# Kernel optimization log

Hardware: AMD Instinct MI355X
Metric: run time of the kernel (lower is better)

The kernel has to match this reference:

```python
import jax, jax.numpy as jnp
import numpy as np

D_MODEL = 1024
NUM_HEADS = 16
D_K = D_MODEL // NUM_HEADS


def setup_inputs() -> dict:
    key = jax.random.key(0)
    ks = jax.random.split(key, 11)
    B, S = 2, 2048
    scale = 1.0 / np.sqrt(D_MODEL)
    inp = {
        'Q': jax.random.normal(ks[0], (B, S, D_MODEL), dtype=jnp.float32),
        'K': jax.random.normal(ks[1], (B, S, D_MODEL), dtype=jnp.float32),
        'V': jax.random.normal(ks[2], (B, S, D_MODEL), dtype=jnp.float32),
        'Wq': jax.random.normal(ks[3], (D_MODEL, D_MODEL), dtype=jnp.float32) * scale,
        'bq': jax.random.normal(ks[4], (D_MODEL,), dtype=jnp.float32) * scale,
        'Wk': jax.random.normal(ks[5], (D_MODEL, D_MODEL), dtype=jnp.float32) * scale,
        'bk': jax.random.normal(ks[6], (D_MODEL,), dtype=jnp.float32) * scale,
        'Wv': jax.random.normal(ks[7], (D_MODEL, D_MODEL), dtype=jnp.float32) * scale,
        'bv': jax.random.normal(ks[8], (D_MODEL,), dtype=jnp.float32) * scale,
        'Wo': jax.random.normal(ks[9], (D_MODEL, D_MODEL), dtype=jnp.float32) * scale,
        'bo': jax.random.normal(ks[10], (D_MODEL,), dtype=jnp.float32) * scale,
    }
    return inp


def _split_heads(x):
    B, S, _ = x.shape
    return x.reshape(B, S, NUM_HEADS, D_K).transpose(0, 2, 1, 3)  # [B,H,S,dk]


def reference(Q, K, V, Wq, bq, Wk, bk, Wv, bv, Wo, bo):
    # Linear projections (torch Linear: x @ W.T + b)
    q = _split_heads(Q @ Wq.T + bq)
    k = _split_heads(K @ Wk.T + bk)
    v = _split_heads(V @ Wv.T + bv)
    scores = jnp.einsum('bhqd,bhkd->bhqk', q, k) / jnp.sqrt(jnp.float32(D_K))
    probs = jax.nn.softmax(scores, axis=-1)
    out = jnp.einsum('bhqk,bhkd->bhqd', probs, v)  # [B,H,S,dk]
    B, H, S, dk = out.shape
    out = out.transpose(0, 2, 1, 3).reshape(B, S, D_MODEL)
    return out @ Wo.T + bo
```

## Files before the change

### kernel.cpp

```cpp
#include <hip/hip_runtime.h>
#include <hip/hip_bf16.h>

#define DEV __device__ __forceinline__

#define BATCH 2
#define SEQ   2048
#define DMODEL 1024
#define NHEAD 16
#define DK    64
#define MROWS (BATCH*SEQ)
#define KD    1024
#define GEMM_NT (KD/32)

#define QSCALE 0.18033688011112042f
#define SMREF  17.312340490667560f

typedef __attribute__((ext_vector_type(4))) float f32x4;
typedef __attribute__((ext_vector_type(8))) short s16x8;
typedef __attribute__((ext_vector_type(4))) short s16x4;
typedef __attribute__((ext_vector_type(4))) float fvec4;

__device__ short g_X[3][MROWS*DMODEL];
__device__ short g_W[4][DMODEL*DMODEL];
__device__ short g_q [MROWS*DMODEL];
__device__ short g_k [MROWS*DMODEL];
__device__ short g_vt[MROWS*DMODEL];
__device__ short g_at[MROWS*DMODEL];

DEV short f2bf(float f) {
  union { __hip_bfloat16 h; short s; } u;
  u.h = __float2bfloat16(f);
  return u.s;
}

DEV void gload_lds16(const void* g, void* l) {
  __builtin_amdgcn_global_load_lds(
      (const __attribute__((address_space(1))) void*)g,
      (__attribute__((address_space(3))) void*)l, 16, 0, 0);
}

__global__ __launch_bounds__(256) void cast3(const float* __restrict__ a,
                                             const float* __restrict__ b,
                                             const float* __restrict__ c, int n8) {
  const float* src = blockIdx.z == 0 ? a : blockIdx.z == 1 ? b : c;
  short* dst = g_X[blockIdx.z];
  int i = blockIdx.x * 256 + threadIdx.x;
  if (i < n8) {
    const fvec4* p = (const fvec4*)(src + (size_t)i*8);
    fvec4 v0 = p[0], v1 = p[1];
    s16x8 r;
    r[0]=f2bf(v0[0]); r[1]=f2bf(v0[1]); r[2]=f2bf(v0[2]); r[3]=f2bf(v0[3]);
    r[4]=f2bf(v1[0]); r[5]=f2bf(v1[1]); r[6]=f2bf(v1[2]); r[7]=f2bf(v1[3]);
    *(s16x8*)(dst + (size_t)i*8) = r;
  }
}

__global__ __launch_bounds__(256) void cast4(const float* __restrict__ a,
                                             const float* __restrict__ b,
                                             const float* __restrict__ c,
                                             const float* __restrict__ d, int n8) {
  const float* src = blockIdx.z == 0 ? a : blockIdx.z == 1 ? b
                   : blockIdx.z == 2 ? c : d;
  short* dst = g_W[blockIdx.z];
  int i = blockIdx.x * 256 + threadIdx.x;
  if (i < n8) {
    const fvec4* p = (const fvec4*)(src + (size_t)i*8);
    fvec4 v0 = p[0], v1 = p[1];
    s16x8 r;
    r[0]=f2bf(v0[0]); r[1]=f2bf(v0[1]); r[2]=f2bf(v0[2]); r[3]=f2bf(v0[3]);
    r[4]=f2bf(v1[0]); r[5]=f2bf(v1[1]); r[6]=f2bf(v1[2]); r[7]=f2bf(v1[3]);
    *(s16x8*)(dst + (size_t)i*8) = r;
  }
}

struct GemmSmem { short As[3][128*32]; short Bs[3][128*32]; };

DEV void gemm_core(GemmSmem& sm, const short* __restrict__ A,
                   const short* __restrict__ Bw, const float* __restrict__ bias,
                   void* __restrict__ outp, float scale, int mode,
                   int rowBase, int colBase) {
  const int t = threadIdx.x, l = t & 63, w = t >> 6, g = l >> 4;
  const int wr = w >> 1, wc = w & 1;

  f32x4 acc[4][4] = {};

  auto stage = [&](int buf, int k0) {
#pragma unroll
    for (int j = 0; j < 2; ++j) {
      int e = w*1024 + j*512 + l*8;
      int e2 = e ^ (((e >> 7) & 3) << 3);
      int r = e2 >> 5, c = e2 & 31;
      gload_lds16(A  + (size_t)(rowBase + r)*KD + k0 + c, &sm.As[buf][w*1024 + j*512]);
      gload_lds16(Bw + (size_t)(colBase + r)*KD + k0 + c, &sm.Bs[buf][w*1024 + j*512]);
    }
  };

  stage(0, 0);
  stage(1, 32);

  int cur = 0, nxt = 2;
  for (int i = 0; i < GEMM_NT; ++i) {
    if (i < GEMM_NT - 1) asm volatile("s_waitcnt vmcnt(4)" ::: "memory");
    else                 asm volatile("s_waitcnt vmcnt(0)" ::: "memory");
    __builtin_amdgcn_s_barrier();
    __builtin_amdgcn_sched_barrier(0);

    s16x8 a[4], b[4];
#pragma unroll
    for (int x = 0; x < 4; ++x) {
      int ra = wr*64 + x*16 + (l & 15);
      int ia = (ra*32 + g*8) ^ (((ra >> 2) & 3) << 3);
      a[x] = *(const s16x8*)&sm.As[cur][ia];
      int rb = wc*64 + x*16 + (l & 15);
      int ib = (rb*32 + g*8) ^ (((rb >> 2) & 3) << 3);
      b[x] = *(const s16x8*)&sm.Bs[cur][ib];
    }
    if (i + 2 < GEMM_NT) stage(nxt, (i + 2)*32);
    __builtin_amdgcn_sched_barrier(0);

    __builtin_amdgcn_s_setprio(1);
#pragma unroll
    for (int x = 0; x < 4; ++x)
#pragma unroll
      for (int jn = 0; jn < 4; ++jn)
        acc[x][jn] = __builtin_amdgcn_mfma_f32_16x16x32_bf16(a[x], b[jn], acc[x][jn], 0, 0, 0);
    __builtin_amdgcn_s_setprio(0);

    cur = cur == 2 ? 0 : cur + 1;
    nxt = nxt == 2 ? 0 : nxt + 1;
  }

#pragma unroll
  for (int x = 0; x < 4; ++x) {
    int mrow0 = rowBase + wr*64 + x*16 + g*4;
#pragma unroll
    for (int jn = 0; jn < 4; ++jn) {
      int n = colBase + wc*64 + jn*16 + (l & 15);
      float bv = bias[n];
#pragma unroll
      for (int r = 0; r < 4; ++r) {
        int m = mrow0 + r;
        float val = (acc[x][jn][r] + bv) * scale;
        if (mode == 1) {
          int b = m >> 11, s = m & 2047, h = n >> 6, d = n & 63;
          ((short*)outp)[(((size_t)(b*NHEAD + h)*SEQ + s)*DK) + d] = f2bf(val);
        } else if (mode == 2) {
          int b = m >> 11, s = m & 2047, h = n >> 6, d = n & 63;
          ((short*)outp)[((size_t)(b*NHEAD + h)*DK + d)*SEQ + s] = f2bf(val);
        } else {
          ((float*)outp)[(size_t)m*DMODEL + n] = val;
        }
      }
    }
  }
}

__global__ __launch_bounds__(256, 3)
void proj_qkv(const float* __restrict__ bq, const float* __restrict__ bk,
              const float* __restrict__ bv) {
  __shared__ GemmSmem sm;
  int z = blockIdx.z;
  int orig = blockIdx.y*8 + blockIdx.x;
  int swz = (orig & 7)*32 + (orig >> 3);
  int bx = swz & 7, by = swz >> 3;
  const float* bias = z == 0 ? bq : z == 1 ? bk : bv;
  void* outp = z == 0 ? (void*)g_q : z == 1 ? (void*)g_k : (void*)g_vt;
  gemm_core(sm, g_X[z], g_W[z], bias, outp, z == 0 ? QSCALE : 1.0f,
            z == 2 ? 2 : 1, by*128, bx*128);
}

__global__ __launch_bounds__(256, 3)
void proj_out(const float* __restrict__ bo, float* __restrict__ out) {
  __shared__ GemmSmem sm;
  int orig = blockIdx.y*8 + blockIdx.x;
  int swz = (orig & 7)*32 + (orig >> 3);
  int bx = swz & 7, by = swz >> 3;
  gemm_core(sm, g_at, g_W[3], bo, out, 1.0f, 3, by*128, bx*128);
}

__global__ __launch_bounds__(256, 4)
void attn_kernel(short* __restrict__ aout) {
  __shared__ short qs[64*64];
  __shared__ short ks[2][64*64];
  __shared__ short vs[2][64*64];

  const int t = threadIdx.x, l = t & 63, w = t >> 6, g = l >> 4;
  const int q15 = l & 15;
  int orig = blockIdx.y*32 + blockIdx.x;
  int swz = (orig & 7)*128 + (orig >> 3);
  const int qblk = swz & 31, bh = swz >> 5;
  const int qbase = qblk * 64;
  const size_t hoff = (size_t)bh * SEQ * DK;

  auto stage_kv = [&](int buf, int kt) {
#pragma unroll
    for (int j = 0; j < 2; ++j) {
      int e = w*1024 + j*512 + l*8;
      int e2 = e ^ (((e >> 6) & 7) << 3);
      gload_lds16(g_k + hoff + (size_t)kt*DK + e2, &ks[buf][w*1024 + j*512]);
      gload_lds16(g_vt + hoff + (size_t)(e2 >> 6)*SEQ + kt + (e2 & 63),
                  &vs[buf][w*1024 + j*512]);
    }
  };

  {
#pragma unroll
    for (int j = 0; j < 2; ++j) {
      int e = w*1024 + j*512 + l*8;
      int e2 = e ^ (((e >> 6) & 7) << 3);
      gload_lds16(g_q + hoff + (size_t)qbase*DK + e2, &qs[w*1024 + j*512]);
    }
    stage_kv(0, 0);
  }
  __syncthreads();

  s16x8 qf[2];
#pragma unroll
  for (int kf = 0; kf < 2; ++kf) {
    int row = w*16 + q15;
    int idx = (row*64 + kf*32 + g*8) ^ ((row & 7) << 3);
    qf[kf] = *(const s16x8*)&qs[idx];
  }

  float lsum = 0.f;
  f32x4 o[4] = {};

  int cur = 0;
  for (int kt = 0; kt < SEQ; kt += 64) {
    if (kt + 64 < SEQ) stage_kv(cur ^ 1, kt + 64);

    f32x4 sc[4] = {};
    __builtin_amdgcn_s_setprio(1);
#pragma unroll
    for (int ni = 0; ni < 4; ++ni)
#pragma unroll
      for (int kf = 0; kf < 2; ++kf) {
        int row = ni*16 + q15;
        int idx = (row*64 + kf*32 + g*8) ^ ((row & 7) << 3);
        s16x8 afr = *(const s16x8*)&ks[cur][idx];
        sc[ni] = __builtin_amdgcn_mfma_f32_16x16x32_bf16(afr, qf[kf], sc[ni], 0, 0, 0);
      }
    __builtin_amdgcn_s_setprio(0);

    float p[4][4];
#pragma unroll
    for (int ni = 0; ni < 4; ++ni)
#pragma unroll
      for (int r = 0; r < 4; ++r)
        p[ni][r] = exp2f(sc[ni][r] - SMREF);

    float s0 = (p[0][0]+p[0][1]) + (p[0][2]+p[0][3]);
    float s1 = (p[1][0]+p[1][1]) + (p[1][2]+p[1][3]);
    float s2 = (p[2][0]+p[2][1]) + (p[2][2]+p[2][3]);
    float s3 = (p[3][0]+p[3][1]) + (p[3][2]+p[3][3]);
    lsum += (s0+s1) + (s2+s3);

#pragma unroll
    for (int ni = 0; ni < 4; ++ni) {
      s16x4 pv;
#pragma unroll
      for (int r = 0; r < 4; ++r) pv[r] = f2bf(p[ni][r]);
      int idx = w*1024 + q15*64 + ((ni*16 + g*4) ^ ((q15 & 7) << 3));
      *(s16x4*)&qs[idx] = pv;
    }

    asm volatile("s_waitcnt lgkmcnt(0)" ::: "memory");
    __builtin_amdgcn_sched_barrier(0);

    s16x8 pa[2];
#pragma unroll
    for (int kf = 0; kf < 2; ++kf) {
      int idx = w*1024 + q15*64 + ((kf*32 + g*8) ^ ((q15 & 7) << 3));
      pa[kf] = *(const s16x8*)&qs[idx];
    }

    __builtin_amdgcn_s_setprio(1);
#pragma unroll
    for (int nd = 0; nd < 4; ++nd)
#pragma unroll
      for (int kf = 0; kf < 2; ++kf) {
        int row = nd*16 + q15;
        int idx = (row*64 + kf*32 + g*8) ^ ((row & 7) << 3);
        s16x8 bfr = *(const s16x8*)&vs[cur][idx];
        o[nd] = __builtin_amdgcn_mfma_f32_16x16x32_bf16(pa[kf], bfr, o[nd], 0, 0, 0);
      }
    __builtin_amdgcn_s_setprio(0);

    asm volatile("s_waitcnt vmcnt(0)" ::: "memory");
    __builtin_amdgcn_s_barrier();
    __builtin_amdgcn_sched_barrier(0);
    cur ^= 1;
  }

  lsum += __shfl_xor(lsum, 16);
  lsum += __shfl_xor(lsum, 32);
  float inv = 1.0f / lsum;
  float iv[4];
#pragma unroll
  for (int r = 0; r < 4; ++r)
    iv[r] = __shfl(inv, (l & 48) | (g*4 + r));

  int b = bh >> 4, h = bh & 15;
#pragma unroll
  for (int nd = 0; nd < 4; ++nd) {
    int dcol = h*DK + nd*16 + q15;
#pragma unroll
    for (int r = 0; r < 4; ++r) {
      int srow = qbase + w*16 + g*4 + r;
      aout[((size_t)(b*SEQ + srow))*DMODEL + dcol] = f2bf(o[nd][r] * iv[r]);
    }
  }
}

extern "C" void kernel_launch(void* const* d_in, const int* in_sizes, int n_in,
                              void* d_out, int out_size, void* d_ws, size_t ws_size,
                              hipStream_t stream) {
  const float* Q  = (const float*)d_in[0];
  const float* K  = (const float*)d_in[1];
  const float* V  = (const float*)d_in[2];
  const float* Wq = (const float*)d_in[3];
  const float* bq = (const float*)d_in[4];
  const float* Wk = (const float*)d_in[5];
  const float* bk = (const float*)d_in[6];
  const float* Wv = (const float*)d_in[7];
  const float* bv = (const float*)d_in[8];
  const float* Wo = (const float*)d_in[9];
  const float* bo = (const float*)d_in[10];

  short* pat;
  hipGetSymbolAddress((void**)&pat, HIP_SYMBOL(g_at));

  const int nX8 = MROWS*DMODEL/8;
  const int nW8 = DMODEL*DMODEL/8;
  dim3 blk(256);

  cast3<<<dim3(nX8/256, 1, 3), blk, 0, stream>>>(Q, K, V, nX8);
  cast4<<<dim3(nW8/256, 1, 4), blk, 0, stream>>>(Wq, Wk, Wv, Wo, nW8);
  proj_qkv<<<dim3(DMODEL/128, MROWS/128, 3), blk, 0, stream>>>(bq, bk, bv);
  attn_kernel<<<dim3(SEQ/64, BATCH*NHEAD), blk, 0, stream>>>(pat);
  proj_out<<<dim3(DMODEL/128, MROWS/128), blk, 0, stream>>>(bo, (float*)d_out);
}
```

Before: 155.0 us.

## Use 8-wave attention blocks with triple-buffered K/V and single barrier per tile

The attention kernel now uses 512-thread blocks covering 128 query rows, so each K/V tile staged in LDS is shared by twice as many waves. K/V staging becomes a three-stage ring: two tiles are prefetched ahead, and each iteration waits with a partial vmcnt, then synchronizes with one barrier. K fragments are loaded into registers before the next tile's async load is issued. Q fragments are read directly from global memory instead of through LDS. This aims to halve K/V global traffic per query and hide load latency, at the cost of more LDS per block and more registers for the K fragments.

```diff
diff --git a/kernel.cpp b/kernel.cpp
--- a/kernel.cpp
+++ b/kernel.cpp
@@ -11,6 +11,7 @@
 #define MROWS (BATCH*SEQ)
 #define KD    1024
 #define GEMM_NT (KD/32)
+#define ATTN_NT (SEQ/64)
 
 #define QSCALE 0.18033688011112042f
 #define SMREF  17.312340490667560f
@@ -178,68 +179,65 @@
   gemm_core(sm, g_at, g_W[3], bo, out, 1.0f, 3, by*128, bx*128);
 }
 
-__global__ __launch_bounds__(256, 4)
+__global__ __launch_bounds__(512, 4)
 void attn_kernel(short* __restrict__ aout) {
-  __shared__ short qs[64*64];
-  __shared__ short ks[2][64*64];
-  __shared__ short vs[2][64*64];
+  __shared__ short ps[128*64];
+  __shared__ short ks[3][64*64];
+  __shared__ short vs[3][64*64];
 
   const int t = threadIdx.x, l = t & 63, w = t >> 6, g = l >> 4;
   const int q15 = l & 15;
-  int orig = blockIdx.y*32 + blockIdx.x;
-  int swz = (orig & 7)*128 + (orig >> 3);
-  const int qblk = swz & 31, bh = swz >> 5;
-  const int qbase = qblk * 64;
+  int orig = blockIdx.y*16 + blockIdx.x;
+  int swz = (orig & 7)*64 + (orig >> 3);
+  const int qblk = swz & 15, bh = swz >> 4;
+  const int qbase = qblk * 128;
   const size_t hoff = (size_t)bh * SEQ * DK;
 
   auto stage_kv = [&](int buf, int kt) {
-#pragma unroll
-    for (int j = 0; j < 2; ++j) {
-      int e = w*1024 + j*512 + l*8;
-      int e2 = e ^ (((e >> 6) & 7) << 3);
-      gload_lds16(g_k + hoff + (size_t)kt*DK + e2, &ks[buf][w*1024 + j*512]);
-      gload_lds16(g_vt + hoff + (size_t)(e2 >> 6)*SEQ + kt + (e2 & 63),
-                  &vs[buf][w*1024 + j*512]);
-    }
+    int e = t*8;
+    int e2 = e ^ (((e >> 6) & 7) << 3);
+    gload_lds16(g_k + hoff + (size_t)kt*DK + e2, &ks[buf][e]);
+    gload_lds16(g_vt + hoff + (size_t)(e2 >> 6)*SEQ + kt + (e2 & 63), &vs[buf][e]);
   };
 
+  s16x8 qf[2];
   {
-#pragma unroll
-    for (int j = 0; j < 2; ++j) {
-      int e = w*1024 + j*512 + l*8;
-      int e2 = e ^ (((e >> 6) & 7) << 3);
-      gload_lds16(g_q + hoff + (size_t)qbase*DK + e2, &qs[w*1024 + j*512]);
-    }
-    stage_kv(0, 0);
-  }
-  __syncthreads();
-
-  s16x8 qf[2];
-#pragma unroll
-  for (int kf = 0; kf < 2; ++kf) {
-    int row = w*16 + q15;
-    int idx = (row*64 + kf*32 + g*8) ^ ((row & 7) << 3);
-    qf[kf] = *(const s16x8*)&qs[idx];
-  }
+    const short* qrow = g_q + hoff + (size_t)(qbase + w*16 + q15)*DK;
+    qf[0] = *(const s16x8*)(qrow + g*8);
+    qf[1] = *(const s16x8*)(qrow + 32 + g*8);
+  }
+  stage_kv(0, 0);
+  stage_kv(1, 64);
 
   float lsum = 0.f;
   f32x4 o[4] = {};
 
-  int cur = 0;
-  for (int kt = 0; kt < SEQ; kt += 64) {
-    if (kt + 64 < SEQ) stage_kv(cur ^ 1, kt + 64);
-
-    f32x4 sc[4] = {};
-    __builtin_amdgcn_s_setprio(1);
+  int cur = 0, nxt = 2;
+  for (int i = 0; i < ATTN_NT; ++i) {
+    if (i < ATTN_NT - 1) asm volatile("s_waitcnt vmcnt(2)" ::: "memory");
+    else                 asm volatile("s_waitcnt vmcnt(0)" ::: "memory");
+    __builtin_amdgcn_s_barrier();
+    __builtin_amdgcn_sched_barrier(0);
+
+    s16x8 kfr[4][2];
 #pragma unroll
     for (int ni = 0; ni < 4; ++ni)
 #pragma unroll
       for (int kf = 0; kf < 2; ++kf) {
         int row = ni*16 + q15;
         int idx = (row*64 + kf*32 + g*8) ^ ((row & 7) << 3);
-        s16x8 afr = *(const s16x8*)&ks[cur][idx];
-        sc[ni] = __builtin_amdgcn_mfma_f32_16x16x32_bf16(afr, qf[kf], sc[ni], 0, 0, 0);
+        kfr[ni][kf] = *(const s16x8*)&ks[cur][idx];
       }
+    if (i + 2 < ATTN_NT) stage_kv(nxt, (i + 2)*64);
+    __builtin_amdgcn_sched_barrier(0);
+
+    f32x4 sc[4] = {};
+    __builtin_amdgcn_s_setprio(1);
+#pragma unroll
+    for (int ni = 0; ni < 4; ++ni)
+#pragma unroll
+      for (int kf = 0; kf < 2; ++kf)
+        sc[ni] = __builtin_amdgcn_mfma_f32_16x16x32_bf16(kfr[ni][kf], qf[kf], sc[ni], 0, 0, 0);
     __builtin_amdgcn_s_setprio(0);
 
     float p[4][4];
@@ -261,7 +259,7 @@
 #pragma unroll
       for (int r = 0; r < 4; ++r) pv[r] = f2bf(p[ni][r]);
       int idx = w*1024 + q15*64 + ((ni*16 + g*4) ^ ((q15 & 7) << 3));
-      *(s16x4*)&qs[idx] = pv;
+      *(s16x4*)&ps[idx] = pv;
     }
 
     asm volatile("s_waitcnt lgkmcnt(0)" ::: "memory");
@@ -271,7 +269,7 @@
 #pragma unroll
     for (int kf = 0; kf < 2; ++kf) {
       int idx = w*1024 + q15*64 + ((kf*32 + g*8) ^ ((q15 & 7) << 3));
-      pa[kf] = *(const s16x8*)&qs[idx];
+      pa[kf] = *(const s16x8*)&ps[idx];
     }
 
     __builtin_amdgcn_s_setprio(1);
@@ -286,10 +284,8 @@
       }
     __builtin_amdgcn_s_setprio(0);
 
-    asm volatile("s_waitcnt vmcnt(0)" ::: "memory");
-    __builtin_amdgcn_s_barrier();
-    __builtin_amdgcn_sched_barrier(0);
-    cur ^= 1;
+    cur = cur == 2 ? 0 : cur + 1;
+    nxt = nxt == 2 ? 0 : nxt + 1;
   }
 
   lsum += __shfl_xor(lsum, 16);
@@ -337,6 +333,6 @@
   cast3<<<dim3(nX8/256, 1, 3), blk, 0, stream>>>(Q, K, V, nX8);
   cast4<<<dim3(nW8/256, 1, 4), blk, 0, stream>>>(Wq, Wk, Wv, Wo, nW8);
   proj_qkv<<<dim3(DMODEL/128, MROWS/128, 3), blk, 0, stream>>>(bq, bk, bv);
-  attn_kernel<<<dim3(SEQ/64, BATCH*NHEAD), blk, 0, stream>>>(pat);
+  attn_kernel<<<dim3(SEQ/128, BATCH*NHEAD), dim3(512), 0, stream>>>(pat);
   proj_out<<<dim3(DMODEL/128, MROWS/128), blk, 0, stream>>>(bo, (float*)d_out);
 }
```

Measured after the change: 147.5 us. -4.9%, faster.
